# Performance work log

Hardware: AMD Instinct MI355X
Metric: run time of the kernel (lower is better)

## Reference

```python
import jax, jax.numpy as jnp
import numpy as np

N, E = 50000, 800000
IN_FEATS, H, L = 16, 64, 3


def _glorot(key, shape):
    fan_in = shape[-1]
    return jax.random.normal(key, shape, dtype=jnp.float32) / np.sqrt(fan_in)


def setup_inputs() -> dict:
    key = jax.random.key(0)
    ks = jax.random.split(key, 12)
    return {
        "features": jax.random.normal(ks[0], (N, IN_FEATS), dtype=jnp.float32),
        "src": jax.random.randint(ks[1], (E,), 0, N, dtype=jnp.int32),
        "dst": jax.random.randint(ks[2], (E,), 0, N, dtype=jnp.int32),
        # input_module: Linear(in_feats, hidden)
        "W_in": _glorot(ks[3], (IN_FEATS, H)),
        "b_in": jnp.zeros((H,), jnp.float32),
        # edge_module: Linear(2*hidden, 1), shared across layers
        "W_edge": _glorot(ks[4], (2 * H, 1)),
        "b_edge": jnp.zeros((1,), jnp.float32),
        # per-layer GRUCell params (torch layout: [3H, H] for W_ih/W_hh)
        "Wih": _glorot(ks[5], (L, 3 * H, H)),
        "Whh": _glorot(ks[6], (L, 3 * H, H)),
        "bih": jnp.zeros((L, 3 * H), jnp.float32),
        "bhh": jnp.zeros((L, 3 * H), jnp.float32),
        # edge_predictor: Linear(2*hidden, 1)
        "W_pred": _glorot(ks[7], (2 * H, 1)),
        "b_pred": jnp.zeros((1,), jnp.float32),
    }


def _gru_cell(x, h, W_ih, W_hh, b_ih, b_hh):
    # torch.nn.GRUCell math
    gi = x @ W_ih.T + b_ih  # [N, 3H]
    gh = h @ W_hh.T + b_hh  # [N, 3H]
    i_r, i_z, i_n = jnp.split(gi, 3, axis=1)
    h_r, h_z, h_n = jnp.split(gh, 3, axis=1)
    r = jax.nn.sigmoid(i_r + h_r)
    z = jax.nn.sigmoid(i_z + h_z)
    n = jnp.tanh(i_n + r * h_n)
    return (1.0 - z) * n + z * h


def reference(features, src, dst, W_in, b_in, W_edge, b_edge, Wih, Whh, bih, bhh, W_pred, b_pred):
    n_nodes = features.shape[0]
    h = features @ W_in + b_in  # [N, H]
    num_layers = Wih.shape[0]
    for l in range(num_layers):
        h_u = h[src]  # [E, H] gather src
        h_v = h[dst]  # [E, H] gather dst
        # shared edge module: sigmoid(Linear(cat[h_u, h_v]))
        w = jax.nn.sigmoid(jnp.concatenate([h_u, h_v], axis=1) @ W_edge + b_edge)  # [E, 1]
        m = h_u * w  # messages [E, H]
        h_new = jax.ops.segment_sum(m, dst, num_segments=n_nodes)  # scatter-sum to dst
        h = _gru_cell(h_new, h, Wih[l], Whh[l], bih[l], bhh[l])
    edges_h = jnp.concatenate([h[src], h[dst]], axis=1)  # [E, 2H]
    return (edges_h @ W_pred + b_pred).squeeze()  # [E]
```

## Files before the change

kernel.cpp:

```cpp
#include <hip/hip_runtime.h>
#include <hip/hip_bf16.h>

#define H 64
#define H3 192
#define ITEMS 16

typedef __attribute__((ext_vector_type(8))) short short8;
typedef __attribute__((ext_vector_type(4))) float f32x4;

__device__ __forceinline__ float sigmoidf_(float x) {
    return 1.0f / (1.0f + __expf(-x));
}
__device__ __forceinline__ float tanhf_(float x) {
    float e = __expf(2.0f * x);
    return 1.0f - 2.0f / (e + 1.0f);
}
__device__ __forceinline__ unsigned short f2bf(float f) {
    unsigned u = __builtin_bit_cast(unsigned, f);
    u += 0x7FFFu + ((u >> 16) & 1u);
    return (unsigned short)(u >> 16);
}
__device__ __forceinline__ float bf2f(unsigned short s) {
    return __builtin_bit_cast(float, (unsigned)s << 16);
}

__global__ __launch_bounds__(256) void input_gates_kernel(
    const float* __restrict__ feat, const float* __restrict__ Win,
    const float* __restrict__ bin, const float* __restrict__ Wg,
    float* __restrict__ h, unsigned short* __restrict__ h_bf,
    float* __restrict__ a_gate, float* __restrict__ b_gate,
    int N)
{
    __shared__ float sWin[16 * H];
    __shared__ float sbin[H];
    __shared__ float sWg[2 * H];
    int t = threadIdx.x;
    for (int i = t; i < 16 * H; i += 256) sWin[i] = Win[i];
    if (t < H) sbin[t] = bin[t];
    if (t < 2 * H) sWg[t] = Wg[t];
    __syncthreads();

    int n = blockIdx.x * 256 + t;
    if (n >= N) return;

    float f[16];
    const float4* fr = (const float4*)(feat + (size_t)n * 16);
#pragma unroll
    for (int i = 0; i < 4; i++) {
        float4 v = fr[i];
        f[4 * i + 0] = v.x; f[4 * i + 1] = v.y; f[4 * i + 2] = v.z; f[4 * i + 3] = v.w;
    }
    float a = 0.f, b = 0.f;
    float* hrow = h + (size_t)n * H;
    unsigned short* brow = h_bf + (size_t)n * H;
    for (int j = 0; j < H; j++) {
        float hj = sbin[j];
#pragma unroll
        for (int k = 0; k < 16; k++) hj += f[k] * sWin[k * H + j];
        hrow[j] = hj;
        brow[j] = f2bf(hj);
        a += hj * sWg[j];
        b += hj * sWg[H + j];
    }
    a_gate[n] = a;
    b_gate[n] = b;
}

__global__ __launch_bounds__(256) void convert_w_kernel(
    const float* __restrict__ Wih, const float* __restrict__ Whh,
    unsigned short* __restrict__ out, int per)
{
    int i = blockIdx.x * 256 + threadIdx.x;
    if (i < per) out[i] = f2bf(Wih[i]);
    else if (i < 2 * per) out[i] = f2bf(Whh[i - per]);
}

__global__ __launch_bounds__(256) void bucket_hist_kernel(
    const int* __restrict__ dst, int* __restrict__ bhist, int E, int nb_c)
{
    __shared__ int lh[256];
    int t = threadIdx.x;
    lh[t] = 0;
    __syncthreads();
    int base = blockIdx.x * (256 * ITEMS);
#pragma unroll
    for (int k = 0; k < ITEMS; k++) {
        int i = base + k * 256 + t;
        if (i < E) atomicAdd(&lh[dst[i] >> 8], 1);
    }
    __syncthreads();
    bhist[t * nb_c + blockIdx.x] = lh[t];
}

__global__ __launch_bounds__(256) void scan_pass1(
    const int* __restrict__ deg, int* __restrict__ locals,
    int* __restrict__ bsum, int N)
{
    int t = threadIdx.x;
    int i = blockIdx.x * 256 + t;
    int v = (i < N) ? deg[i] : 0;
    int lane = t & 63, w = t >> 6;
    int s = v;
#pragma unroll
    for (int off = 1; off < 64; off <<= 1) {
        int u = __shfl_up(s, off);
        if (lane >= off) s += u;
    }
    __shared__ int wsum[4];
    if (lane == 63) wsum[w] = s;
    __syncthreads();
    int add = 0;
    for (int k = 0; k < w; k++) add += wsum[k];
    if (i < N) locals[i] = s + add - v;
    if (t == 255) bsum[blockIdx.x] = s + add;
}

__global__ __launch_bounds__(1024) void scan_pass2(
    const int* __restrict__ bsum, int* __restrict__ carry, int nb)
{
    __shared__ int sums[1024];
    int t = threadIdx.x;
    int chunk = (nb + 1023) >> 10;
    int beg = t * chunk;
    int end = beg + chunk; if (end > nb) end = nb;
    if (beg > nb) beg = nb;
    int s = 0;
    for (int i = beg; i < end; i++) s += bsum[i];
    sums[t] = s;
    __syncthreads();
    for (int off = 1; off < 1024; off <<= 1) {
        int v = (t >= off) ? sums[t - off] : 0;
        __syncthreads();
        sums[t] += v;
        __syncthreads();
    }
    int prefix = (t == 0) ? 0 : sums[t - 1];
    for (int i = beg; i < end; i++) { carry[i] = prefix; prefix += bsum[i]; }
}

__global__ __launch_bounds__(256) void scan_pass3b(
    const int* __restrict__ locals, const int* __restrict__ carry,
    int* __restrict__ S, int M, int E)
{
    int i = blockIdx.x * 256 + threadIdx.x;
    if (i < M) S[i] = locals[i] + carry[blockIdx.x];
    else if (i == M) S[M] = E;
}

__global__ __launch_bounds__(256) void bucket_scatter_kernel(
    const int* __restrict__ src, const int* __restrict__ dst,
    const int* __restrict__ S, unsigned* __restrict__ pk, int E, int nb_c)
{
    __shared__ int lbase[256];
    __shared__ int lrun[256];
    int t = threadIdx.x;
    lbase[t] = S[t * nb_c + blockIdx.x];
    lrun[t] = 0;
    __syncthreads();
    int base = blockIdx.x * (256 * ITEMS);
#pragma unroll
    for (int k = 0; k < ITEMS; k++) {
        int i = base + k * 256 + t;
        if (i < E) {
            int d = dst[i];
            int b = d >> 8;
            int r = atomicAdd(&lrun[b], 1);
            pk[lbase[b] + r] = ((unsigned)(d & 255) << 16) | (unsigned)src[i];
        }
    }
}

__global__ __launch_bounds__(256) void bucket_finalize_kernel(
    const unsigned* __restrict__ pk, const int* __restrict__ S,
    int* __restrict__ offsets, unsigned short* __restrict__ csr16,
    int N, int E, int nb_c, int NB)
{
    __shared__ int lh[256];
    __shared__ int loff[256];
    __shared__ int lrun[256];
    int t = threadIdx.x;
    int b = blockIdx.x;
    int beg = S[b * nb_c];
    int endb = (b + 1 < NB) ? S[(b + 1) * nb_c] : E;
    lh[t] = 0; lrun[t] = 0;
    __syncthreads();
    for (int i = beg + t; i < endb; i += 256) atomicAdd(&lh[pk[i] >> 16], 1);
    __syncthreads();
    int v = lh[t];
    loff[t] = v;
    __syncthreads();
    for (int off = 1; off < 256; off <<= 1) {
        int u = (t >= off) ? loff[t - off] : 0;
        __syncthreads();
        loff[t] += u;
        __syncthreads();
    }
    int excl = loff[t] - v;
    int node = b * 256 + t;
    if (node < N) offsets[node] = beg + excl;
    if (b == NB - 1 && t == 0) offsets[N] = E;
    loff[t] = excl;
    __syncthreads();
    for (int i = beg + t; i < endb; i += 256) {
        unsigned w = pk[i];
        int d = (int)(w >> 16);
        int r = atomicAdd(&lrun[d], 1);
        csr16[beg + loff[d] + r] = (unsigned short)(w & 0xFFFFu);
    }
}

__global__ __launch_bounds__(256) void aggregate_kernel(
    const unsigned short* __restrict__ h_bf, const float* __restrict__ a_gate,
    const float* __restrict__ b_gate, const int* __restrict__ offsets,
    const unsigned short* __restrict__ csr16, const float* __restrict__ b_edge,
    unsigned short* __restrict__ hnew_bf, int N)
{
    int wid = threadIdx.x >> 6;
    int lane = threadIdx.x & 63;
    int sub = lane >> 3;
    int cg  = lane & 7;
    int v = blockIdx.x * 4 + wid;
    if (v >= N) return;

    int beg = offsets[v];
    int end = offsets[v + 1];
    float bv = b_gate[v] + b_edge[0];
    float acc[8] = {0.f, 0.f, 0.f, 0.f, 0.f, 0.f, 0.f, 0.f};

    for (int cs = beg; cs < end; cs += 64) {
        int m = end - cs; if (m > 64) m = 64;
        int u = 0; float w = 0.f;
        if (lane < m) {
            u = (int)csr16[cs + lane];
            w = sigmoidf_(a_gate[u] + bv);
        }
        for (int j = 0; j < m; j += 8) {
            int e = j + sub;
            int uj = __shfl(u, e & 63);
            float wj = __shfl(w, e & 63);
            if (e >= m) wj = 0.f;
            short8 hv = *(const short8*)(h_bf + (size_t)uj * H + cg * 8);
#pragma unroll
            for (int k = 0; k < 8; k++)
                acc[k] += wj * bf2f((unsigned short)hv[k]);
        }
    }
#pragma unroll
    for (int mm = 8; mm < 64; mm <<= 1) {
#pragma unroll
        for (int k = 0; k < 8; k++)
            acc[k] += __shfl_xor(acc[k], mm);
    }
    if (sub == 0) {
        short8 o;
#pragma unroll
        for (int k = 0; k < 8; k++) o[k] = (short)f2bf(acc[k]);
        *(short8*)(hnew_bf + (size_t)v * H + cg * 8) = o;
    }
}

__global__ __launch_bounds__(256) void gru_mfma_kernel(
    const unsigned short* __restrict__ x_bf,
    float* __restrict__ h,
    unsigned short* __restrict__ h_bf,
    const unsigned short* __restrict__ wih_bf,
    const unsigned short* __restrict__ whh_bf,
    const float* __restrict__ bih, const float* __restrict__ bhh,
    const float* __restrict__ Wg,
    float* __restrict__ a_gate, float* __restrict__ b_gate, int N)
{
    int lane = threadIdx.x & 63;
    int wv = threadIdx.x >> 6;
    int c = lane & 15;
    int g = lane >> 4;
    int nbase = blockIdx.x * 64 + wv * 16;
    if (nbase >= N) return;

    int nrow = nbase + c;
    int nclamp = nrow < N ? nrow : (N - 1);

    short8 ax[2], ah[2];
#pragma unroll
    for (int ch = 0; ch < 2; ch++) {
        ax[ch] = *(const short8*)(x_bf + (size_t)nclamp * H + ch * 32 + g * 8);
        ah[ch] = *(const short8*)(h_bf + (size_t)nclamp * H + ch * 32 + g * 8);
    }

    f32x4 gi[12], gh[12];
#pragma unroll
    for (int jb = 0; jb < 12; jb++) {
        gi[jb] = (f32x4){0.f, 0.f, 0.f, 0.f};
        gh[jb] = (f32x4){0.f, 0.f, 0.f, 0.f};
    }

#pragma unroll
    for (int jb = 0; jb < 12; jb++) {
        const unsigned short* wi = wih_bf + (size_t)(jb * 16 + c) * H + g * 8;
        const unsigned short* wh = whh_bf + (size_t)(jb * 16 + c) * H + g * 8;
        short8 wi0 = *(const short8*)(wi);
        short8 wi1 = *(const short8*)(wi + 32);
        short8 wh0 = *(const short8*)(wh);
        short8 wh1 = *(const short8*)(wh + 32);
        gi[jb] = __builtin_amdgcn_mfma_f32_16x16x32_bf16(ax[0], wi0, gi[jb], 0, 0, 0);
        gi[jb] = __builtin_amdgcn_mfma_f32_16x16x32_bf16(ax[1], wi1, gi[jb], 0, 0, 0);
        gh[jb] = __builtin_amdgcn_mfma_f32_16x16x32_bf16(ah[0], wh0, gh[jb], 0, 0, 0);
        gh[jb] = __builtin_amdgcn_mfma_f32_16x16x32_bf16(ah[1], wh1, gh[jb], 0, 0, 0);
    }

    float pa[4] = {0.f, 0.f, 0.f, 0.f};
    float pb[4] = {0.f, 0.f, 0.f, 0.f};
#pragma unroll
    for (int jb = 0; jb < 4; jb++) {
        int j = jb * 16 + c;
        float br = bih[j] + bhh[j];
        float bz = bih[H + j] + bhh[H + j];
        float bin_ = bih[2 * H + j];
        float bhn_ = bhh[2 * H + j];
        float wga = Wg[j], wgb = Wg[H + j];
#pragma unroll
        for (int q = 0; q < 4; q++) {
            int node = nbase + g * 4 + q;
            float r = sigmoidf_(gi[jb][q] + gh[jb][q] + br);
            float z = sigmoidf_(gi[jb + 4][q] + gh[jb + 4][q] + bz);
            float nn = tanhf_(gi[jb + 8][q] + bin_ + r * (gh[jb + 8][q] + bhn_));
            size_t idx = (size_t)node * H + j;
            float hp = h[idx];
            float ho = (1.0f - z) * nn + z * hp;
            h[idx] = ho;
            h_bf[idx] = f2bf(ho);
            pa[q] += ho * wga;
            pb[q] += ho * wgb;
        }
    }
#pragma unroll
    for (int m = 1; m < 16; m <<= 1) {
#pragma unroll
        for (int q = 0; q < 4; q++) {
            pa[q] += __shfl_xor(pa[q], m);
            pb[q] += __shfl_xor(pb[q], m);
        }
    }
    if (c == 0) {
#pragma unroll
        for (int q = 0; q < 4; q++) {
            int node = nbase + g * 4 + q;
            a_gate[node] = pa[q];
            b_gate[node] = pb[q];
        }
    }
}

__global__ __launch_bounds__(256) void predict_kernel(
    const int* __restrict__ src, const int* __restrict__ dst,
    const float* __restrict__ pa, const float* __restrict__ pb,
    const float* __restrict__ b_pred, float* __restrict__ out, int E)
{
    int e4 = (blockIdx.x * 256 + threadIdx.x) * 4;
    float bp = b_pred[0];
    if (e4 + 3 < E) {
        int4 s = *(const int4*)(src + e4);
        int4 d = *(const int4*)(dst + e4);
        float4 o;
        o.x = pa[s.x] + pb[d.x] + bp;
        o.y = pa[s.y] + pb[d.y] + bp;
        o.z = pa[s.z] + pb[d.z] + bp;
        o.w = pa[s.w] + pb[d.w] + bp;
        *(float4*)(out + e4) = o;
    } else {
        for (int e = e4; e < E; e++)
            out[e] = pa[src[e]] + pb[dst[e]] + bp;
    }
}

extern "C" void kernel_launch(void* const* d_in, const int* in_sizes, int n_in,
                              void* d_out, int out_size, void* d_ws, size_t ws_size,
                              hipStream_t stream) {
    const float* features = (const float*)d_in[0];
    const int*   src      = (const int*)d_in[1];
    const int*   dst      = (const int*)d_in[2];
    const float* W_in     = (const float*)d_in[3];
    const float* b_in     = (const float*)d_in[4];
    const float* W_edge   = (const float*)d_in[5];
    const float* b_edge   = (const float*)d_in[6];
    const float* Wih      = (const float*)d_in[7];
    const float* Whh      = (const float*)d_in[8];
    const float* bih      = (const float*)d_in[9];
    const float* bhh      = (const float*)d_in[10];
    const float* W_pred   = (const float*)d_in[11];
    const float* b_pred   = (const float*)d_in[12];
    float* out = (float*)d_out;

    int N = in_sizes[0] / 16;
    int E = in_sizes[1];
    int L = in_sizes[7] / (H3 * H);
    int per = L * H3 * H;

    int nb_nodes = (N + 255) / 256;
    int nb_agg   = (N + 3) / 4;
    int nb_gru   = (N + 63) / 64;
    int nb_conv  = (2 * per + 255) / 256;
    int nb_pred  = (E + 1023) / 1024;

    int nb_c = (E + 256 * ITEMS - 1) / (256 * ITEMS);
    int NB   = (N + 255) / 256;
    int M    = 256 * nb_c;
    int mb   = (M + 255) / 256;
    int nb_s3 = (M + 1 + 255) / 256;

    float* h = (float*)d_ws;
    unsigned short* h_bf = (unsigned short*)(h + (size_t)N * H);
    unsigned short* hnew_bf = h_bf + (size_t)N * H;
    unsigned short* w_bf = hnew_bf + (size_t)N * H;
    float* a_gate = (float*)(w_bf + 2 * per);
    float* b_gate = a_gate + N;
    int* offsets  = (int*)(b_gate + N);
    unsigned* pk  = (unsigned*)(offsets + N + 1);
    unsigned short* csr16 = (unsigned short*)(pk + E);
    int* bhist = (int*)(csr16 + E);
    int* bloc  = bhist + M;
    int* sbh   = bloc + M;
    int* bsum  = sbh + M + 1;
    int* carry = bsum + mb;

    input_gates_kernel<<<nb_nodes, 256, 0, stream>>>(
        features, W_in, b_in, W_edge, h, h_bf, a_gate, b_gate, N);
    convert_w_kernel<<<nb_conv, 256, 0, stream>>>(Wih, Whh, w_bf, per);

    bucket_hist_kernel<<<nb_c, 256, 0, stream>>>(dst, bhist, E, nb_c);
    scan_pass1<<<mb, 256, 0, stream>>>(bhist, bloc, bsum, M);
    scan_pass2<<<1, 1024, 0, stream>>>(bsum, carry, mb);
    scan_pass3b<<<nb_s3, 256, 0, stream>>>(bloc, carry, sbh, M, E);
    bucket_scatter_kernel<<<nb_c, 256, 0, stream>>>(src, dst, sbh, pk, E, nb_c);
    bucket_finalize_kernel<<<NB, 256, 0, stream>>>(pk, sbh, offsets, csr16, N, E, nb_c, NB);

    for (int l = 0; l < L; l++) {
        aggregate_kernel<<<nb_agg, 256, 0, stream>>>(
            h_bf, a_gate, b_gate, offsets, csr16, b_edge, hnew_bf, N);
        const float* Wg = (l < L - 1) ? W_edge : W_pred;
        gru_mfma_kernel<<<nb_gru, 256, 0, stream>>>(
            hnew_bf, h, h_bf,
            w_bf + (size_t)l * H3 * H,
            w_bf + (size_t)per + (size_t)l * H3 * H,
            bih + (size_t)l * H3, bhh + (size_t)l * H3,
            Wg, a_gate, b_gate, N);
    }

    predict_kernel<<<nb_pred, 256, 0, stream>>>(src, dst, a_gate, b_gate, b_pred, out, E);
}
```

Measured before the change: 260.3 us.

## Merge setup kernels, fold scan carry pass, double gathers in aggregate

Fuses the input projection, weight conversion and bucket histogram into a single launch that dispatches on block index, removing two kernel launches. Replaces the single-block carry scan and the add pass with one kernel where each block sums the preceding block totals itself. The aggregate loop now processes two edge groups per iteration with separate accumulators, so more gathers are in flight. The trade-offs are redundant summation of block totals in every scan block and higher register pressure in aggregate.

Measured after the change: 247.1 us. -5.1%, faster.

```diff
diff --git a/kernel.cpp b/kernel.cpp
--- a/kernel.cpp
+++ b/kernel.cpp
@@ -24,72 +24,69 @@
     return __builtin_bit_cast(float, (unsigned)s << 16);
 }
 
-__global__ __launch_bounds__(256) void input_gates_kernel(
+__global__ __launch_bounds__(256) void setup_kernel(
     const float* __restrict__ feat, const float* __restrict__ Win,
     const float* __restrict__ bin, const float* __restrict__ Wg,
     float* __restrict__ h, unsigned short* __restrict__ h_bf,
     float* __restrict__ a_gate, float* __restrict__ b_gate,
-    int N)
-{
-    __shared__ float sWin[16 * H];
-    __shared__ float sbin[H];
-    __shared__ float sWg[2 * H];
+    const float* __restrict__ Wih, const float* __restrict__ Whh,
+    unsigned short* __restrict__ w_bf,
+    const int* __restrict__ dst, int* __restrict__ bhist,
+    int N, int E, int per, int nbA, int nbB, int nb_c)
+{
+    int bid = blockIdx.x;
     int t = threadIdx.x;
-    for (int i = t; i < 16 * H; i += 256) sWin[i] = Win[i];
-    if (t < H) sbin[t] = bin[t];
-    if (t < 2 * H) sWg[t] = Wg[t];
-    __syncthreads();
-
-    int n = blockIdx.x * 256 + t;
-    if (n >= N) return;
-
-    float f[16];
-    const float4* fr = (const float4*)(feat + (size_t)n * 16);
-#pragma unroll
-    for (int i = 0; i < 4; i++) {
-        float4 v = fr[i];
-        f[4 * i + 0] = v.x; f[4 * i + 1] = v.y; f[4 * i + 2] = v.z; f[4 * i + 3] = v.w;
-    }
-    float a = 0.f, b = 0.f;
-    float* hrow = h + (size_t)n * H;
-    unsigned short* brow = h_bf + (size_t)n * H;
-    for (int j = 0; j < H; j++) {
-        float hj = sbin[j];
-#pragma unroll
-        for (int k = 0; k < 16; k++) hj += f[k] * sWin[k * H + j];
-        hrow[j] = hj;
-        brow[j] = f2bf(hj);
-        a += hj * sWg[j];
-        b += hj * sWg[H + j];
-    }
-    a_gate[n] = a;
-    b_gate[n] = b;
-}
-
-__global__ __launch_bounds__(256) void convert_w_kernel(
-    const float* __restrict__ Wih, const float* __restrict__ Whh,
-    unsigned short* __restrict__ out, int per)
-{
-    int i = blockIdx.x * 256 + threadIdx.x;
-    if (i < per) out[i] = f2bf(Wih[i]);
-    else if (i < 2 * per) out[i] = f2bf(Whh[i - per]);
-}
-
-__global__ __launch_bounds__(256) void bucket_hist_kernel(
-    const int* __restrict__ dst, int* __restrict__ bhist, int E, int nb_c)
-{
-    __shared__ int lh[256];
-    int t = threadIdx.x;
-    lh[t] = 0;
-    __syncthreads();
-    int base = blockIdx.x * (256 * ITEMS);
-#pragma unroll
-    for (int k = 0; k < ITEMS; k++) {
-        int i = base + k * 256 + t;
-        if (i < E) atomicAdd(&lh[dst[i] >> 8], 1);
-    }
-    __syncthreads();
-    bhist[t * nb_c + blockIdx.x] = lh[t];
+    if (bid < nbA) {
+        __shared__ float sWin[16 * H];
+        __shared__ float sbin[H];
+        __shared__ float sWg[2 * H];
+        for (int i = t; i < 16 * H; i += 256) sWin[i] = Win[i];
+        if (t < H) sbin[t] = bin[t];
+        if (t < 2 * H) sWg[t] = Wg[t];
+        __syncthreads();
+
+        int n = bid * 256 + t;
+        if (n >= N) return;
+
+        float f[16];
+        const float4* fr = (const float4*)(feat + (size_t)n * 16);
+#pragma unroll
+        for (int i = 0; i < 4; i++) {
+            float4 v = fr[i];
+            f[4 * i + 0] = v.x; f[4 * i + 1] = v.y;
+            f[4 * i + 2] = v.z; f[4 * i + 3] = v.w;
+        }
+        float a = 0.f, b = 0.f;
+        float* hrow = h + (size_t)n * H;
+        unsigned short* brow = h_bf + (size_t)n * H;
+        for (int j = 0; j < H; j++) {
+            float hj = sbin[j];
+#pragma unroll
+            for (int k = 0; k < 16; k++) hj += f[k] * sWin[k * H + j];
+            hrow[j] = hj;
+            brow[j] = f2bf(hj);
+            a += hj * sWg[j];
+            b += hj * sWg[H + j];
+        }
+        a_gate[n] = a;
+        b_gate[n] = b;
+    } else if (bid < nbA + nbB) {
+        int i = (bid - nbA) * 256 + t;
+        if (i < per) w_bf[i] = f2bf(Wih[i]);
+        else if (i < 2 * per) w_bf[i] = f2bf(Whh[i - per]);
+    } else {
+        __shared__ int lh[256];
+        lh[t] = 0;
+        __syncthreads();
+        int base = (bid - nbA - nbB) * (256 * ITEMS);
+#pragma unroll
+        for (int k = 0; k < ITEMS; k++) {
+            int i = base + k * 256 + t;
+            if (i < E) atomicAdd(&lh[dst[i] >> 8], 1);
+        }
+        __syncthreads();
+        bhist[t * nb_c + (bid - nbA - nbB)] = lh[t];
+    }
 }
 
 __global__ __launch_bounds__(256) void scan_pass1(
@@ -115,35 +112,23 @@
     if (t == 255) bsum[blockIdx.x] = s + add;
 }
 
-__global__ __launch_bounds__(1024) void scan_pass2(
-    const int* __restrict__ bsum, int* __restrict__ carry, int nb)
-{
-    __shared__ int sums[1024];
+__global__ __launch_bounds__(256) void scan_pass3c(
+    const int* __restrict__ locals, const int* __restrict__ bsum,
+    int* __restrict__ S, int M, int E, int mb)
+{
     int t = threadIdx.x;
-    int chunk = (nb + 1023) >> 10;
-    int beg = t * chunk;
-    int end = beg + chunk; if (end > nb) end = nb;
-    if (beg > nb) beg = nb;
-    int s = 0;
-    for (int i = beg; i < end; i++) s += bsum[i];
-    sums[t] = s;
-    __syncthreads();
-    for (int off = 1; off < 1024; off <<= 1) {
-        int v = (t >= off) ? sums[t - off] : 0;
-        __syncthreads();
-        sums[t] += v;
-        __syncthreads();
-    }
-    int prefix = (t == 0) ? 0 : sums[t - 1];
-    for (int i = beg; i < end; i++) { carry[i] = prefix; prefix += bsum[i]; }
-}
-
-__global__ __launch_bounds__(256) void scan_pass3b(
-    const int* __restrict__ locals, const int* __restrict__ carry,
-    int* __restrict__ S, int M, int E)
-{
-    int i = blockIdx.x * 256 + threadIdx.x;
-    if (i < M) S[i] = locals[i] + carry[blockIdx.x];
+    int b = blockIdx.x;
+    int v = 0;
+    for (int k = t; k < b && k < mb; k += 256) v += bsum[k];
+#pragma unroll
+    for (int off = 32; off >= 1; off >>= 1) v += __shfl_xor(v, off);
+    __shared__ int ws[4];
+    if ((t & 63) == 0) ws[t >> 6] = v;
+    __syncthreads();
+    int carry = ws[0] + ws[1] + ws[2] + ws[3];
+
+    int i = b * 256 + t;
+    if (i < M) S[i] = locals[i] + carry;
     else if (i == M) S[M] = E;
 }
 
@@ -225,7 +210,8 @@
     int beg = offsets[v];
     int end = offsets[v + 1];
     float bv = b_gate[v] + b_edge[0];
-    float acc[8] = {0.f, 0.f, 0.f, 0.f, 0.f, 0.f, 0.f, 0.f};
+    float acc0[8] = {0.f, 0.f, 0.f, 0.f, 0.f, 0.f, 0.f, 0.f};
+    float acc1[8] = {0.f, 0.f, 0.f, 0.f, 0.f, 0.f, 0.f, 0.f};
 
     for (int cs = beg; cs < end; cs += 64) {
         int m = end - cs; if (m > 64) m = 64;
@@ -234,27 +220,36 @@
             u = (int)csr16[cs + lane];
             w = sigmoidf_(a_gate[u] + bv);
         }
-        for (int j = 0; j < m; j += 8) {
-            int e = j + sub;
-            int uj = __shfl(u, e & 63);
-            float wj = __shfl(w, e & 63);
-            if (e >= m) wj = 0.f;
-            short8 hv = *(const short8*)(h_bf + (size_t)uj * H + cg * 8);
+        for (int j = 0; j < m; j += 16) {
+            int e0 = j + sub, e1 = j + 8 + sub;
+            int u0 = __shfl(u, e0 & 63);
+            float w0 = __shfl(w, e0 & 63);
+            int u1 = __shfl(u, e1 & 63);
+            float w1 = __shfl(w, e1 & 63);
+            if (e0 >= m) w0 = 0.f;
+            if (e1 >= m) w1 = 0.f;
+            short8 hv0 = *(const short8*)(h_bf + (size_t)u0 * H + cg * 8);
+            short8 hv1 = *(const short8*)(h_bf + (size_t)u1 * H + cg * 8);
 #pragma unroll
             for (int k = 0; k < 8; k++)
-                acc[k] += wj * bf2f((unsigned short)hv[k]);
-        }
-    }
+                acc0[k] += w0 * bf2f((unsigned short)hv0[k]);
+#pragma unroll
+            for (int k = 0; k < 8; k++)
+                acc1[k] += w1 * bf2f((unsigned short)hv1[k]);
+        }
+    }
+#pragma unroll
+    for (int k = 0; k < 8; k++) acc0[k] += acc1[k];
 #pragma unroll
     for (int mm = 8; mm < 64; mm <<= 1) {
 #pragma unroll
         for (int k = 0; k < 8; k++)
-            acc[k] += __shfl_xor(acc[k], mm);
+            acc0[k] += __shfl_xor(acc0[k], mm);
     }
     if (sub == 0) {
         short8 o;
 #pragma unroll
-        for (int k = 0; k < 8; k++) o[k] = (short)f2bf(acc[k]);
+        for (int k = 0; k < 8; k++) o[k] = (short)f2bf(acc0[k]);
         *(short8*)(hnew_bf + (size_t)v * H + cg * 8) = o;
     }
 }
@@ -420,16 +415,14 @@
     int* bloc  = bhist + M;
     int* sbh   = bloc + M;
     int* bsum  = sbh + M + 1;
-    int* carry = bsum + mb;
-
-    input_gates_kernel<<<nb_nodes, 256, 0, stream>>>(
-        features, W_in, b_in, W_edge, h, h_bf, a_gate, b_gate, N);
-    convert_w_kernel<<<nb_conv, 256, 0, stream>>>(Wih, Whh, w_bf, per);
-
-    bucket_hist_kernel<<<nb_c, 256, 0, stream>>>(dst, bhist, E, nb_c);
+
+    setup_kernel<<<nb_nodes + nb_conv + nb_c, 256, 0, stream>>>(
+        features, W_in, b_in, W_edge, h, h_bf, a_gate, b_gate,
+        Wih, Whh, w_bf, dst, bhist,
+        N, E, per, nb_nodes, nb_conv, nb_c);
+
     scan_pass1<<<mb, 256, 0, stream>>>(bhist, bloc, bsum, M);
-    scan_pass2<<<1, 1024, 0, stream>>>(bsum, carry, mb);
-    scan_pass3b<<<nb_s3, 256, 0, stream>>>(bloc, carry, sbh, M, E);
+    scan_pass3c<<<nb_s3, 256, 0, stream>>>(bloc, bsum, sbh, M, E, mb);
     bucket_scatter_kernel<<<nb_c, 256, 0, stream>>>(src, dst, sbh, pk, E, nb_c);
     bucket_finalize_kernel<<<NB, 256, 0, stream>>>(pk, sbh, offsets, csr16, N, E, nb_c, NB);
 
```
